# Performance work log

Measured on AMD Instinct MI355X. Metric: run time of the kernel, lower is better.

Reference implementation:

```python
import jax, jax.numpy as jnp
import numpy as np

IN_CAPS, IN_DIMS = 32, 288
OUT_CAPS, OUT_DIMS = 10, 16
N_ITERS = 3


def setup_inputs() -> dict:
    key = jax.random.key(0)
    k1, k2 = jax.random.split(key)
    B = 8192
    data = jax.random.normal(k1, (B, IN_CAPS, IN_DIMS), dtype=jnp.float32)
    stdv = 1.0 / 32.0
    W = jax.random.uniform(k2, (IN_CAPS, IN_DIMS, OUT_CAPS * OUT_DIMS),
                           dtype=jnp.float32, minval=-stdv, maxval=stdv)
    return {"data": data, "W": W}


def reference(data, W):
    B = data.shape[0]
    # u_hat[b,i,o,d]: per-input-capsule predictions for each output capsule
    u_hat = jnp.einsum('bci,cio->bco', data, W).reshape(B, IN_CAPS, OUT_CAPS, OUT_DIMS)
    b = jnp.zeros((IN_CAPS, OUT_CAPS), dtype=u_hat.dtype)
    v = None
    for _ in range(N_ITERS):  # fixed small iteration count
        c = jax.nn.softmax(b, axis=0)                      # (IN_CAPS, OUT_CAPS), softmax over input capsules
        v = jnp.einsum('io,biod->bod', c, u_hat)           # (B, OUT_CAPS, OUT_DIMS)
        # agreement: sqrt of sum of squared elementwise products, averaged over batch
        a = jnp.sqrt(jnp.sum((u_hat * v[:, None, :, :]) ** 2, axis=-1)).mean(axis=0)
        b = b + a
    return v
```

## Files before the change

### kernel.cpp

```cpp
#include <hip/hip_runtime.h>
#include <hip/hip_bf16.h>

#define NB 8192
#define IC 32
#define ID 288
#define OD16 160

typedef __attribute__((ext_vector_type(8))) short bf16x8;
typedef __attribute__((ext_vector_type(4))) float f32x4;

__device__ __forceinline__ unsigned short f2bf(float f) {
    unsigned int u = __builtin_bit_cast(unsigned int, f);
    u = u + 0x7fffu + ((u >> 16) & 1u);
    return (unsigned short)(u >> 16);
}
__device__ __forceinline__ float bf2f(unsigned short h) {
    return __builtin_bit_cast(float, ((unsigned int)h) << 16);
}
__device__ __forceinline__ bf16x8 cvt_bf8(const f32x4& a, const f32x4& b) {
    union { __hip_bfloat162 h[4]; bf16x8 v; } u;
    u.h[0] = __float22bfloat162_rn(make_float2(a[0], a[1]));
    u.h[1] = __float22bfloat162_rn(make_float2(a[2], a[3]));
    u.h[2] = __float22bfloat162_rn(make_float2(b[0], b[1]));
    u.h[3] = __float22bfloat162_rn(make_float2(b[2], b[3]));
    return u.v;
}

__device__ __forceinline__ void gld_lds16(const void* g, void* l) {
    __builtin_amdgcn_global_load_lds((const __attribute__((address_space(1))) unsigned int*)g,
                                     (__attribute__((address_space(3))) unsigned int*)l, 16, 0, 0);
}

__global__ __launch_bounds__(256) void prep_kernel(const float* __restrict__ W,
                                                   unsigned short* __restrict__ Bimg,
                                                   float* __restrict__ a_arr) {
    __shared__ short tile[160 * 72];
    const int bx = blockIdx.x;
    const int c = bx / 5;
    const int s = bx - c * 5;
    const int t = threadIdx.x;
    if (bx == 0) {
        for (int i = t; i < 3 * 8 * 320; i += 256) a_arr[i] = 0.f;
    }
    const int kw = (s == 4) ? 32 : 64;
    const int nel = kw * 160;
    for (int idx = t; idx < nel; idx += 256) {
        int k = idx / 160;
        int n = idx - k * 160;
        tile[n * 72 + k] = (short)f2bf(W[((long)c * ID + s * 64 + k) * OD16 + n]);
    }
    __syncthreads();
    unsigned short* dst0 = Bimg + ((long)c * 9 + s * 2) * (160 * 32);
    const int nkc = (s == 4) ? 1 : 2;
    for (int kcl = 0; kcl < nkc; ++kcl) {
        unsigned short* dst = dst0 + kcl * (160 * 32);
        for (int p = t; p < 640; p += 256) {
            int n = p >> 2;
            int sl = p & 3;
            int g = sl ^ ((n >> 1) & 3);
            *(uint4*)(dst + p * 8) = *(const uint4*)&tile[n * 72 + kcl * 32 + g * 8];
        }
    }
}

__global__ __launch_bounds__(256) void gemm_kernel(const float* __restrict__ data,
                                                   const unsigned short* __restrict__ Bimg,
                                                   unsigned short* __restrict__ uhat) {
    __shared__ alignas(16) char lds[53248];
    char* const Alds = lds;
    char* const Blds = lds + 32768;
    const int tid = threadIdx.x;
    const int lane = tid & 63;
    const int w = tid >> 6;
    const int q = lane >> 4;
    const int r = lane & 15;
    const int b0 = blockIdx.x * 128;
    const int cc = blockIdx.y;

    const float* Ag = data + (long)(b0 + w * 32 + (lane >> 3)) * (IC * ID) + cc * ID
                      + ((lane & 7) ^ ((lane >> 3) & 7)) * 4;
    const unsigned short* Bc = Bimg + (long)cc * (9 * 160 * 32);

    f32x4 acc[2][10];
    #pragma unroll
    for (int i = 0; i < 2; ++i)
        #pragma unroll
        for (int j = 0; j < 10; ++j)
            acc[i][j] = (f32x4){0.f, 0.f, 0.f, 0.f};

    auto issueA = [&](int buf, int kc) {
        char* dst = Alds + w * 8192 + buf * 4096;
        const float* src = Ag + kc * 32;
        #pragma unroll
        for (int j = 0; j < 4; ++j)
            gld_lds16(src + (long)j * 8 * (IC * ID), dst + j * 1024);
    };
    auto issueB = [&](int buf, int kc) {
        const unsigned short* src = Bc + kc * (160 * 32) + (w * 160 + lane) * 8;
        char* dst = Blds + buf * 10240 + w * 2560;
        gld_lds16(src, dst);
        gld_lds16(src + 64 * 8, dst + 1024);
        if (lane < 32) gld_lds16(src + 128 * 8, dst + 2048);
    };

#define COMPUTE(KC)                                                            \
    {                                                                          \
        const char* Ab = Alds + w * 8192 + ((KC) & 1) * 4096;                  \
        const char* Bb = Blds + ((KC) & 1) * 10240;                            \
        const int slot = q ^ ((r >> 1) & 3);                                   \
        bf16x8 bfr[10];                                                        \
        _Pragma("unroll")                                                      \
        for (int nf = 0; nf < 10; ++nf)                                        \
            bfr[nf] = *(const bf16x8*)(Bb + (nf * 16 + r) * 64 + slot * 16);   \
        bf16x8 af[2];                                                          \
        _Pragma("unroll")                                                      \
        for (int mf = 0; mf < 2; ++mf) {                                       \
            const int row = mf * 16 + r;                                       \
            const int c0 = (q * 2) ^ (r & 7);                                  \
            const int c1 = (q * 2 + 1) ^ (r & 7);                              \
            f32x4 alo = *(const f32x4*)(Ab + row * 128 + c0 * 16);             \
            f32x4 ahi = *(const f32x4*)(Ab + row * 128 + c1 * 16);             \
            af[mf] = cvt_bf8(alo, ahi);                                        \
        }                                                                      \
        _Pragma("unroll")                                                      \
        for (int nf = 0; nf < 10; ++nf) {                                      \
            acc[0][nf] = __builtin_amdgcn_mfma_f32_16x16x32_bf16(af[0], bfr[nf], acc[0][nf], 0, 0, 0); \
            acc[1][nf] = __builtin_amdgcn_mfma_f32_16x16x32_bf16(af[1], bfr[nf], acc[1][nf], 0, 0, 0); \
        }                                                                      \
    }

#define WAITV(N)  { asm volatile("s_waitcnt vmcnt(" N ")" ::: "memory");       \
                    __builtin_amdgcn_sched_barrier(0); }
#define BAR()     { __builtin_amdgcn_s_barrier(); }

    issueA(0, 0); issueB(0, 0); issueA(1, 1); issueB(1, 1);
    WAITV("7") BAR() COMPUTE(0) BAR()
    issueA(0, 2); issueB(0, 2); WAITV("7") BAR() COMPUTE(1) BAR()
    issueA(1, 3); issueB(1, 3); WAITV("7") BAR() COMPUTE(2) BAR()
    issueA(0, 4); issueB(0, 4); WAITV("7") BAR() COMPUTE(3) BAR()
    issueA(1, 5); issueB(1, 5); WAITV("7") BAR() COMPUTE(4) BAR()
    issueA(0, 6); issueB(0, 6); WAITV("7") BAR() COMPUTE(5) BAR()
    issueA(1, 7); issueB(1, 7); WAITV("7") BAR() COMPUTE(6) BAR()
    issueA(0, 8); issueB(0, 8); WAITV("7") BAR() COMPUTE(7)
    WAITV("0") BAR() COMPUTE(8)

#undef COMPUTE
#undef WAITV
#undef BAR

    __syncthreads();
    short* eb = (short*)lds;
    #pragma unroll
    for (int mf = 0; mf < 2; ++mf)
        #pragma unroll
        for (int rr = 0; rr < 4; ++rr) {
            const int m = w * 32 + mf * 16 + (q << 2) + rr;
            #pragma unroll
            for (int nf = 0; nf < 10; ++nf)
                eb[m * 168 + nf * 16 + r] = (short)f2bf(acc[mf][nf][rr]);
        }
    __syncthreads();
    unsigned short* dstc = uhat + ((long)cc * NB + b0) * 160;
    #pragma unroll
    for (int j = 0; j < 10; ++j) {
        const int chunk = j * 256 + tid;
        const int row = chunk / 20;
        const int p = chunk - row * 20;
        *(uint4*)(dstc + (long)row * 160 + p * 8) = *(const uint4*)(eb + row * 168 + p * 8);
    }
}

template <int COMPUTE_A, int WRITE_V>
__global__ __launch_bounds__(256) void route_kernel(const unsigned short* __restrict__ uhat,
                                                    const float* __restrict__ a_all,
                                                    int n_prev,
                                                    float* __restrict__ a_out,
                                                    float* __restrict__ v_out) {
    constexpr long PL = (long)NB * 160;
    __shared__ float c_sh[320];
    __shared__ float v_lds[4][160];
    __shared__ float a_sh[4][320];
    const int tid = threadIdx.x;
    for (int base = 0; base < 320; base += 256) {
        int t = base + tid;
        if (t < 320) {
            float bv = 0.f;
            for (int j = 0; j < n_prev * 8; ++j) bv += a_all[j * 320 + t];
            bv *= (1.0f / 8192.0f);
            float m = bv;
            #pragma unroll
            for (int off = 1; off < 32; off <<= 1) m = fmaxf(m, __shfl_xor(m, off));
            float e = __expf(bv - m);
            float ssum = e;
            #pragma unroll
            for (int off = 1; off < 32; off <<= 1) ssum += __shfl_xor(ssum, off);
            c_sh[t] = e / ssum;
        }
    }
    __syncthreads();

    const int w = tid >> 6;
    const int lane = tid & 63;
    const long row = (long)blockIdx.x * 4 + w;
    const unsigned short* __restrict__ u = uhat + row * 160;

    ushort4 ua[5][4];
    if (COMPUTE_A) {
        #pragma unroll
        for (int s5 = 0; s5 < 5; ++s5) {
            const int i = lane & 31;
            const int oo = (lane >> 5) + 2 * s5;
            #pragma unroll
            for (int d4 = 0; d4 < 4; ++d4)
                ua[s5][d4] = *(const ushort4*)(u + (long)i * PL + oo * 16 + d4 * 4);
        }
    }

    if (lane < 40) {
        const int q = lane;
        const int o = q >> 2;
        float4 sv = {0.f, 0.f, 0.f, 0.f};
        #pragma unroll 8
        for (int i = 0; i < 32; ++i) {
            ushort4 uu = *(const ushort4*)(u + (long)i * PL + q * 4);
            float ci = c_sh[o * 32 + i];
            sv.x += ci * bf2f(uu.x);
            sv.y += ci * bf2f(uu.y);
            sv.z += ci * bf2f(uu.z);
            sv.w += ci * bf2f(uu.w);
        }
        if (WRITE_V) *(float4*)(v_out + row * 160 + q * 4) = sv;
        if (COMPUTE_A) *(float4*)(&v_lds[w][q * 4]) = sv;
    }

    if (COMPUTE_A) {
        asm volatile("s_waitcnt lgkmcnt(0)" ::: "memory");
        #pragma unroll
        for (int s5 = 0; s5 < 5; ++s5) {
            const int i = lane & 31;
            const int oo = (lane >> 5) + 2 * s5;
            const float* vp = &v_lds[w][oo * 16];
            float accv = 0.f;
            #pragma unroll
            for (int d4 = 0; d4 < 4; ++d4) {
                ushort4 uu = ua[s5][d4];
                float4 vv = *(const float4*)(vp + d4 * 4);
                float p0 = bf2f(uu.x) * vv.x;
                float p1 = bf2f(uu.y) * vv.y;
                float p2 = bf2f(uu.z) * vv.z;
                float p3 = bf2f(uu.w) * vv.w;
                accv += p0 * p0 + p1 * p1 + p2 * p2 + p3 * p3;
            }
            a_sh[w][oo * 32 + i] = sqrtf(accv);
        }
        __syncthreads();
        for (int t = tid; t < 320; t += 256) {
            float s4 = a_sh[0][t] + a_sh[1][t] + a_sh[2][t] + a_sh[3][t];
            atomicAdd(a_out + (blockIdx.x & 7) * 320 + t, s4);
        }
    }
}

extern "C" void kernel_launch(void* const* d_in, const int* in_sizes, int n_in,
                              void* d_out, int out_size, void* d_ws, size_t ws_size,
                              hipStream_t stream) {
    const float* data = (const float*)d_in[0];
    const float* W = (const float*)d_in[1];
    float* out = (float*)d_out;
    char* ws = (char*)d_ws;

    unsigned short* uhat = (unsigned short*)ws;
    size_t off = (size_t)NB * IC * OD16 * 2;
    unsigned short* Bimg = (unsigned short*)(ws + off);
    off += 32L * 9 * 160 * 32 * 2;
    float* a_arr = (float*)(ws + off); off += 3 * 8 * 320 * 4;

    hipLaunchKernelGGL(prep_kernel, dim3(160), dim3(256), 0, stream, W, Bimg, a_arr);
    hipLaunchKernelGGL(gemm_kernel, dim3(64, 32), dim3(256), 0, stream, data, Bimg, uhat);
    hipLaunchKernelGGL((route_kernel<1, 0>), dim3(2048), dim3(256), 0, stream,
                       uhat, a_arr, 0, a_arr + 0 * 2560, out);
    hipLaunchKernelGGL((route_kernel<1, 0>), dim3(2048), dim3(256), 0, stream,
                       uhat, a_arr, 1, a_arr + 1 * 2560, out);
    hipLaunchKernelGGL((route_kernel<0, 1>), dim3(2048), dim3(256), 0, stream,
                       uhat, a_arr, 2, a_arr + 2 * 2560, out);
}
```

Before: 164.9 us.

## Load whole A row-tile into LDS upfront with contiguous rows, halve M tile

The GEMM block now covers 64 batch rows instead of 128. Each wave loads its 16 full rows of 288 floats into LDS in one contiguous prologue, using a padded row stride of 1168 bytes, rather than double-buffering 32-column chunks. Only the W tiles remain pipelined. The grid is reordered so capsule index is the fast dimension, which is meant to give more contiguous global reads of data and twice as many blocks. The cost is a larger LDS footprint of 96KB, which limits occupancy, and one A fragment per wave, which halves MFMA reuse of each B fragment.

```diff
diff --git a/kernel.cpp b/kernel.cpp
--- a/kernel.cpp
+++ b/kernel.cpp
@@ -66,35 +66,36 @@
 __global__ __launch_bounds__(256) void gemm_kernel(const float* __restrict__ data,
                                                    const unsigned short* __restrict__ Bimg,
                                                    unsigned short* __restrict__ uhat) {
-    __shared__ alignas(16) char lds[53248];
+    __shared__ alignas(16) char lds[98304];
     char* const Alds = lds;
-    char* const Blds = lds + 32768;
+    char* const Blds = lds + 77824;
     const int tid = threadIdx.x;
     const int lane = tid & 63;
     const int w = tid >> 6;
     const int q = lane >> 4;
     const int r = lane & 15;
-    const int b0 = blockIdx.x * 128;
-    const int cc = blockIdx.y;
-
-    const float* Ag = data + (long)(b0 + w * 32 + (lane >> 3)) * (IC * ID) + cc * ID
-                      + ((lane & 7) ^ ((lane >> 3) & 7)) * 4;
+    const int cc = blockIdx.x;
+    const int b0 = blockIdx.y * 64;
+
+    const float* Abase = data + (long)(b0 + w * 16) * (IC * ID) + cc * ID;
     const unsigned short* Bc = Bimg + (long)cc * (9 * 160 * 32);
 
-    f32x4 acc[2][10];
+    f32x4 acc[10];
     #pragma unroll
-    for (int i = 0; i < 2; ++i)
-        #pragma unroll
-        for (int j = 0; j < 10; ++j)
-            acc[i][j] = (f32x4){0.f, 0.f, 0.f, 0.f};
-
-    auto issueA = [&](int buf, int kc) {
-        char* dst = Alds + w * 8192 + buf * 4096;
-        const float* src = Ag + kc * 32;
-        #pragma unroll
-        for (int j = 0; j < 4; ++j)
-            gld_lds16(src + (long)j * 8 * (IC * ID), dst + j * 1024);
-    };
+    for (int j = 0; j < 10; ++j) acc[j] = (f32x4){0.f, 0.f, 0.f, 0.f};
+
+    {
+        char* Adst = Alds + w * 19456;
+        #pragma unroll
+        for (int j = 0; j < 19; ++j) {
+            unsigned n = j * 64 + lane;
+            unsigned rw = (n * 919300u) >> 26;
+            unsigned cg = n - rw * 73;
+            rw = (rw > 15u) ? 15u : rw;
+            cg = (cg > 71u) ? 71u : cg;
+            gld_lds16(Abase + (long)rw * (IC * ID) + cg * 4, Adst + j * 1024);
+        }
+    }
     auto issueB = [&](int buf, int kc) {
         const unsigned short* src = Bc + kc * (160 * 32) + (w * 160 + lane) * 8;
         char* dst = Blds + buf * 10240 + w * 2560;
@@ -105,43 +106,35 @@
 
 #define COMPUTE(KC)                                                            \
     {                                                                          \
-        const char* Ab = Alds + w * 8192 + ((KC) & 1) * 4096;                  \
+        const char* Ab = Alds + w * 19456;                                     \
         const char* Bb = Blds + ((KC) & 1) * 10240;                            \
         const int slot = q ^ ((r >> 1) & 3);                                   \
         bf16x8 bfr[10];                                                        \
         _Pragma("unroll")                                                      \
         for (int nf = 0; nf < 10; ++nf)                                        \
             bfr[nf] = *(const bf16x8*)(Bb + (nf * 16 + r) * 64 + slot * 16);   \
-        bf16x8 af[2];                                                          \
+        f32x4 alo = *(const f32x4*)(Ab + r * 1168 + (KC) * 128 + q * 32);      \
+        f32x4 ahi = *(const f32x4*)(Ab + r * 1168 + (KC) * 128 + q * 32 + 16); \
+        bf16x8 af = cvt_bf8(alo, ahi);                                         \
         _Pragma("unroll")                                                      \
-        for (int mf = 0; mf < 2; ++mf) {                                       \
-            const int row = mf * 16 + r;                                       \
-            const int c0 = (q * 2) ^ (r & 7);                                  \
-            const int c1 = (q * 2 + 1) ^ (r & 7);                              \
-            f32x4 alo = *(const f32x4*)(Ab + row * 128 + c0 * 16);             \
-            f32x4 ahi = *(const f32x4*)(Ab + row * 128 + c1 * 16);             \
-            af[mf] = cvt_bf8(alo, ahi);                                        \
-        }                                                                      \
-        _Pragma("unroll")                                                      \
-        for (int nf = 0; nf < 10; ++nf) {                                      \
-            acc[0][nf] = __builtin_amdgcn_mfma_f32_16x16x32_bf16(af[0], bfr[nf], acc[0][nf], 0, 0, 0); \
-            acc[1][nf] = __builtin_amdgcn_mfma_f32_16x16x32_bf16(af[1], bfr[nf], acc[1][nf], 0, 0, 0); \
-        }                                                                      \
+        for (int nf = 0; nf < 10; ++nf)                                        \
+            acc[nf] = __builtin_amdgcn_mfma_f32_16x16x32_bf16(af, bfr[nf], acc[nf], 0, 0, 0); \
     }
 
 #define WAITV(N)  { asm volatile("s_waitcnt vmcnt(" N ")" ::: "memory");       \
                     __builtin_amdgcn_sched_barrier(0); }
 #define BAR()     { __builtin_amdgcn_s_barrier(); }
 
-    issueA(0, 0); issueB(0, 0); issueA(1, 1); issueB(1, 1);
-    WAITV("7") BAR() COMPUTE(0) BAR()
-    issueA(0, 2); issueB(0, 2); WAITV("7") BAR() COMPUTE(1) BAR()
-    issueA(1, 3); issueB(1, 3); WAITV("7") BAR() COMPUTE(2) BAR()
-    issueA(0, 4); issueB(0, 4); WAITV("7") BAR() COMPUTE(3) BAR()
-    issueA(1, 5); issueB(1, 5); WAITV("7") BAR() COMPUTE(4) BAR()
-    issueA(0, 6); issueB(0, 6); WAITV("7") BAR() COMPUTE(5) BAR()
-    issueA(1, 7); issueB(1, 7); WAITV("7") BAR() COMPUTE(6) BAR()
-    issueA(0, 8); issueB(0, 8); WAITV("7") BAR() COMPUTE(7)
+    issueB(0, 0); issueB(1, 1);
+
+    WAITV("3") BAR() COMPUTE(0) BAR() issueB(0, 2);
+    WAITV("3") BAR() COMPUTE(1) BAR() issueB(1, 3);
+    WAITV("3") BAR() COMPUTE(2) BAR() issueB(0, 4);
+    WAITV("3") BAR() COMPUTE(3) BAR() issueB(1, 5);
+    WAITV("3") BAR() COMPUTE(4) BAR() issueB(0, 6);
+    WAITV("3") BAR() COMPUTE(5) BAR() issueB(1, 7);
+    WAITV("3") BAR() COMPUTE(6) BAR() issueB(0, 8);
+    WAITV("3") BAR() COMPUTE(7) BAR()
     WAITV("0") BAR() COMPUTE(8)
 
 #undef COMPUTE
@@ -151,18 +144,16 @@
     __syncthreads();
     short* eb = (short*)lds;
     #pragma unroll
-    for (int mf = 0; mf < 2; ++mf)
-        #pragma unroll
-        for (int rr = 0; rr < 4; ++rr) {
-            const int m = w * 32 + mf * 16 + (q << 2) + rr;
-            #pragma unroll
-            for (int nf = 0; nf < 10; ++nf)
-                eb[m * 168 + nf * 16 + r] = (short)f2bf(acc[mf][nf][rr]);
-        }
+    for (int rr = 0; rr < 4; ++rr) {
+        const int m = w * 16 + (q << 2) + rr;
+        #pragma unroll
+        for (int nf = 0; nf < 10; ++nf)
+            eb[m * 168 + nf * 16 + r] = (short)f2bf(acc[nf][rr]);
+    }
     __syncthreads();
     unsigned short* dstc = uhat + ((long)cc * NB + b0) * 160;
     #pragma unroll
-    for (int j = 0; j < 10; ++j) {
+    for (int j = 0; j < 5; ++j) {
         const int chunk = j * 256 + tid;
         const int row = chunk / 20;
         const int p = chunk - row * 20;
@@ -276,7 +267,7 @@
     float* a_arr = (float*)(ws + off); off += 3 * 8 * 320 * 4;
 
     hipLaunchKernelGGL(prep_kernel, dim3(160), dim3(256), 0, stream, W, Bimg, a_arr);
-    hipLaunchKernelGGL(gemm_kernel, dim3(64, 32), dim3(256), 0, stream, data, Bimg, uhat);
+    hipLaunchKernelGGL(gemm_kernel, dim3(32, 128), dim3(256), 0, stream, data, Bimg, uhat);
     hipLaunchKernelGGL((route_kernel<1, 0>), dim3(2048), dim3(256), 0, stream,
                        uhat, a_arr, 0, a_arr + 0 * 2560, out);
     hipLaunchKernelGGL((route_kernel<1, 0>), dim3(2048), dim3(256), 0, stream,
```

Measured after the change: 202.8 us. +23.0%, slower.
